# Optimization experiments

Hardware: AMD Instinct MI355X
Metric: run time of the kernel (lower is better)

The kernel has to match this reference:

```python
import jax, jax.numpy as jnp
import numpy as np

B, C, LEN_TS = 4096, 8, 1024
DIM = 2               # shapelet_info[5]
START, END = 0, 628   # max(100-128,0), min(500+128,1024)
L = 64                # len_shapelet
E = 128               # shape_embed_dim
NORM = 1000.0
MAX_CI = 3.0


def setup_inputs() -> dict:
    key = jax.random.key(0)
    k = jax.random.split(key, 6)
    x = jax.random.normal(k[0], (B, C, LEN_TS), dtype=jnp.float32)
    shapelet = jax.random.normal(k[1], (L,), dtype=jnp.float32)
    W1 = jax.random.normal(k[2], (E, L), dtype=jnp.float32) * 0.1
    b1 = jax.random.normal(k[3], (E,), dtype=jnp.float32) * 0.1
    W2 = jax.random.normal(k[4], (E, L), dtype=jnp.float32) * 0.1
    b2 = jax.random.normal(k[5], (E,), dtype=jnp.float32) * 0.1
    return {"x": x, "shapelet": shapelet, "W1": W1, "b1": b1, "W2": W2, "b2": b2}


def reference(x, shapelet, W1, b1, W2, b2):
    piss = x[:, DIM, START:END]                      # [B, T], T = 628
    T = END - START
    NW = T - L + 1                                   # 565 windows

    # squared first differences, then sliding sums of length L-1 via cumsum
    d2 = jnp.square(piss[:, 1:] - piss[:, :-1])      # [B, T-1]
    cs = jnp.concatenate([jnp.zeros((piss.shape[0], 1), piss.dtype),
                          jnp.cumsum(d2, axis=1)], axis=1)   # [B, T]
    piss_ci = jnp.sqrt(cs[:, L - 1:] - cs[:, :NW] + 1.0 / NORM)  # [B, NW]

    # shapelet complexity (constant at init in torch: computed with numpy)
    s_ci = jax.lax.stop_gradient(
        jnp.sqrt(jnp.sum(jnp.square(shapelet[1:] - shapelet[:-1])) + 1.0 / NORM))

    CF = jnp.minimum(jnp.maximum(piss_ci, s_ci) / jnp.minimum(piss_ci, s_ci), MAX_CI)

    # sliding windows [B, NW, L]
    idx = jnp.arange(NW)[:, None] + jnp.arange(L)[None, :]
    piss_w = piss[:, idx]

    ED = jnp.sqrt(jnp.sum(jnp.square(piss_w - shapelet[None, None, :]), axis=-1))  # [B, NW]
    CID = ED * CF

    index = jnp.argmin(CID, axis=1)                  # [B]
    out_i = jnp.take_along_axis(piss_w, index[:, None, None], axis=1)[:, 0, :]  # [B, L]

    out_i = out_i @ W1.T + b1                        # [B, E]
    out_s = shapelet @ W2.T + b2                     # [E]
    out = out_i - out_s[None, :]
    return out.reshape(piss.shape[0], 1, -1)
```

## Files before the change

kernel.cpp:

```cpp
#include <hip/hip_runtime.h>
#include <math.h>

#define NB      4096
#define T       628
#define LW      64
#define NW      565
#define EW      128
#define XSTRIDE 8192
#define XOFF    2048
#define WPT     5

#define WS_SCI 128
#define WS_SS2 129
#define WS_W1T 132
#define WS_NEEDED ((WS_W1T + EW * LW) * sizeof(float))

__global__ __launch_bounds__(64) void prep_kernel(
        const float* __restrict__ shapelet,
        const float* __restrict__ b1,
        const float* __restrict__ W1,
        const float* __restrict__ W2,
        const float* __restrict__ b2,
        float* __restrict__ ws, int use_wt) {
    const int b = blockIdx.x;
    const int j = threadIdx.x;
    const float sh = shapelet[j];
    if (b < EW) {
        const int e = b;
        float dot = sh * W2[e * LW + j];
        #pragma unroll
        for (int off = 32; off; off >>= 1) dot += __shfl_xor(dot, off, 64);
        if (use_wt) ws[WS_W1T + j * EW + e] = W1[e * LW + j];
        if (j == 0) ws[e] = b1[e] - (dot + b2[e]);
    } else {
        float shn = __shfl_down(sh, 1, 64);
        float d = (j < LW - 1) ? (shn - sh) * (shn - sh) : 0.f;
        float q = sh * sh;
        #pragma unroll
        for (int off = 32; off; off >>= 1) {
            d += __shfl_xor(d, off, 64);
            q += __shfl_xor(q, off, 64);
        }
        if (j == 0) { ws[WS_SCI] = sqrtf(d + 0.001f); ws[WS_SS2] = q; }
    }
}

__global__ __launch_bounds__(128, 8) void shapeblock_kernel(
        const float* __restrict__ x,
        const float* __restrict__ shapelet,
        const float* __restrict__ W1,
        const float* __restrict__ ws,
        float* __restrict__ out, int use_wt) {
    __shared__ __align__(16) float sp[T];
    __shared__ unsigned long long red[2];

    const int b   = blockIdx.x;
    const int tid = threadIdx.x;

    const float4* xr4 = (const float4*)(x + (size_t)b * XSTRIDE + XOFF);
    float4* sp4 = (float4*)sp;
    sp4[tid] = xr4[tid];
    if (tid < T / 4 - 128) sp4[tid + 128] = xr4[tid + 128];
    const float s_ci = ws[WS_SCI];
    const float ss2  = ws[WS_SS2];
    __syncthreads();

    const int w0 = (tid * WPT < NW) ? tid * WPT : 0;

    float ring[WPT], acc[WPT], head[WPT];
    #pragma unroll
    for (int i = 0; i < WPT; ++i) {
        ring[i] = sp[w0 + i];
        head[i] = ring[i];
        acc[i]  = 0.f;
    }
    float sd = 0.f, sw2 = 0.f, prev = 0.f;
    #pragma unroll
    for (int j = 0; j < LW; ++j) {
        const float sj = shapelet[j];
        const float v  = ring[j % WPT];
        sw2 = fmaf(v, v, sw2);
        if (j > 0) { float d = v - prev; sd = fmaf(d, d, sd); }
        prev = v;
        #pragma unroll
        for (int i = 0; i < WPT; ++i)
            acc[i] = fmaf(ring[(j + i) % WPT], sj, acc[i]);
        if (j < LW - 1) ring[j % WPT] = sp[w0 + j + WPT];
    }

    unsigned long long key = ~0ull;
    #pragma unroll
    for (int k = 0; k < WPT; ++k) {
        const int w = w0 + k;
        float pci = sqrtf(sd + 0.001f);
        float ed  = sqrtf(fmaxf(fmaf(-2.f, acc[k], sw2 + ss2), 0.f));
        float cf  = fminf(fmaxf(pci, s_ci) / fminf(pci, s_ci), 3.0f);
        float cid = ed * cf;
        unsigned long long kk =
            ((unsigned long long)__float_as_uint(cid) << 32) | (unsigned)w;
        key = kk < key ? kk : key;
        if (k < WPT - 1) {
            float dold = head[k + 1] - head[k];
            float dnew = ring[(4 + k) % WPT] - ring[(3 + k) % WPT];
            sd  = fmaf(dnew, dnew, fmaf(-dold, dold, sd));
            float vold = head[k], vnew = ring[(4 + k) % WPT];
            sw2 = fmaf(vnew, vnew, fmaf(-vold, vold, sw2));
        }
    }

    #pragma unroll
    for (int off = 32; off; off >>= 1) {
        unsigned long long o =
            (unsigned long long)__shfl_xor((long long)key, off, 64);
        key = o < key ? o : key;
    }
    if ((tid & 63) == 0) red[tid >> 6] = key;
    __syncthreads();
    unsigned long long k0 = red[0], k1 = red[1];
    const int widx = (int)((k0 < k1 ? k0 : k1) & 0xffffffffu);

    float a0 = ws[tid];
    if (use_wt) {
        const float* wt = ws + WS_W1T;
        #pragma unroll
        for (int j = 0; j < LW; ++j)
            a0 = fmaf(sp[widx + j], wt[j * EW + tid], a0);
    } else {
        #pragma unroll
        for (int j = 0; j < LW; ++j)
            a0 = fmaf(sp[widx + j], W1[tid * LW + j], a0);
    }
    out[(size_t)b * EW + tid] = a0;
}

extern "C" void kernel_launch(void* const* d_in, const int* in_sizes, int n_in,
                              void* d_out, int out_size, void* d_ws, size_t ws_size,
                              hipStream_t stream) {
    const float* x        = (const float*)d_in[0];
    const float* shapelet = (const float*)d_in[1];
    const float* W1       = (const float*)d_in[2];
    const float* b1       = (const float*)d_in[3];
    const float* W2       = (const float*)d_in[4];
    const float* b2       = (const float*)d_in[5];
    float* out = (float*)d_out;
    float* ws  = (float*)d_ws;

    const int use_wt = (ws_size >= WS_NEEDED) ? 1 : 0;

    prep_kernel<<<EW + 1, 64, 0, stream>>>(shapelet, b1, W1, W2, b2, ws, use_wt);
    shapeblock_kernel<<<NB, 128, 0, stream>>>(x, shapelet, W1, ws, out, use_wt);
}
```

Measured before the change: 25.93 us.

## Fuse prep kernel into main kernel and process two rows per block

Removes the separate prep kernel: each block now computes the shapelet complexity and squared norm in registers, and one half of the block computes the W2·shapelet bias term while the other half does the W1 projection. Blocks grow to 256 threads and handle two batch rows, so the W1 row loaded as float4 is reused for both rows. This drops one kernel launch and the workspace round-trip. In exchange, every block redoes the W2 dot products, and W1 is read in its untransposed layout, which is strided across threads.

```diff
diff --git a/kernel.cpp b/kernel.cpp
--- a/kernel.cpp
+++ b/kernel.cpp
@@ -10,67 +10,49 @@
 #define XOFF    2048
 #define WPT     5
 
-#define WS_SCI 128
-#define WS_SS2 129
-#define WS_W1T 132
-#define WS_NEEDED ((WS_W1T + EW * LW) * sizeof(float))
-
-__global__ __launch_bounds__(64) void prep_kernel(
-        const float* __restrict__ shapelet,
-        const float* __restrict__ b1,
-        const float* __restrict__ W1,
-        const float* __restrict__ W2,
-        const float* __restrict__ b2,
-        float* __restrict__ ws, int use_wt) {
-    const int b = blockIdx.x;
-    const int j = threadIdx.x;
-    const float sh = shapelet[j];
-    if (b < EW) {
-        const int e = b;
-        float dot = sh * W2[e * LW + j];
-        #pragma unroll
-        for (int off = 32; off; off >>= 1) dot += __shfl_xor(dot, off, 64);
-        if (use_wt) ws[WS_W1T + j * EW + e] = W1[e * LW + j];
-        if (j == 0) ws[e] = b1[e] - (dot + b2[e]);
-    } else {
-        float shn = __shfl_down(sh, 1, 64);
-        float d = (j < LW - 1) ? (shn - sh) * (shn - sh) : 0.f;
-        float q = sh * sh;
-        #pragma unroll
-        for (int off = 32; off; off >>= 1) {
-            d += __shfl_xor(d, off, 64);
-            q += __shfl_xor(q, off, 64);
-        }
-        if (j == 0) { ws[WS_SCI] = sqrtf(d + 0.001f); ws[WS_SS2] = q; }
-    }
-}
-
-__global__ __launch_bounds__(128, 8) void shapeblock_kernel(
+__global__ __launch_bounds__(256, 8) void shapeblock_fused(
         const float* __restrict__ x,
         const float* __restrict__ shapelet,
         const float* __restrict__ W1,
-        const float* __restrict__ ws,
-        float* __restrict__ out, int use_wt) {
-    __shared__ __align__(16) float sp[T];
-    __shared__ unsigned long long red[2];
+        const float* __restrict__ b1,
+        const float* __restrict__ W2,
+        const float* __restrict__ b2,
+        float* __restrict__ out) {
+    __shared__ __align__(16) float sp[2][T];
+    __shared__ unsigned long long red[4];
+    __shared__ float s2dot[EW];
 
-    const int b   = blockIdx.x;
-    const int tid = threadIdx.x;
+    const int tid  = threadIdx.x;
+    const int half = tid >> 7;
+    const int l    = tid & 127;
+    const int lane = tid & 63;
+    const int row0 = blockIdx.x * 2;
 
-    const float4* xr4 = (const float4*)(x + (size_t)b * XSTRIDE + XOFF);
-    float4* sp4 = (float4*)sp;
-    sp4[tid] = xr4[tid];
-    if (tid < T / 4 - 128) sp4[tid + 128] = xr4[tid + 128];
-    const float s_ci = ws[WS_SCI];
-    const float ss2  = ws[WS_SS2];
+    const float4* xr4 = (const float4*)(x + (size_t)(row0 + half) * XSTRIDE + XOFF);
+    float4* sp4 = (float4*)sp[half];
+    sp4[l] = xr4[l];
+    if (l < T / 4 - 128) sp4[l + 128] = xr4[l + 128];
+
+    const float shv = shapelet[lane];
+    float shn = __shfl_down(shv, 1, 64);
+    float dsum = (lane < LW - 1) ? (shn - shv) * (shn - shv) : 0.f;
+    float qsum = shv * shv;
+    #pragma unroll
+    for (int off = 32; off; off >>= 1) {
+        dsum += __shfl_xor(dsum, off, 64);
+        qsum += __shfl_xor(qsum, off, 64);
+    }
+    const float s_ci = sqrtf(dsum + 0.001f);
+    const float ss2  = qsum;
     __syncthreads();
 
-    const int w0 = (tid * WPT < NW) ? tid * WPT : 0;
+    const float* mysp = sp[half];
+    const int w0 = (l * WPT < NW) ? l * WPT : 0;
 
     float ring[WPT], acc[WPT], head[WPT];
     #pragma unroll
     for (int i = 0; i < WPT; ++i) {
-        ring[i] = sp[w0 + i];
+        ring[i] = mysp[w0 + i];
         head[i] = ring[i];
         acc[i]  = 0.f;
     }
@@ -85,7 +67,7 @@
         #pragma unroll
         for (int i = 0; i < WPT; ++i)
             acc[i] = fmaf(ring[(j + i) % WPT], sj, acc[i]);
-        if (j < LW - 1) ring[j % WPT] = sp[w0 + j + WPT];
+        if (j < LW - 1) ring[j % WPT] = mysp[w0 + j + WPT];
     }
 
     unsigned long long key = ~0ull;
@@ -114,23 +96,49 @@
             (unsigned long long)__shfl_xor((long long)key, off, 64);
         key = o < key ? o : key;
     }
-    if ((tid & 63) == 0) red[tid >> 6] = key;
+    if (lane == 0) red[tid >> 6] = key;
     __syncthreads();
-    unsigned long long k0 = red[0], k1 = red[1];
-    const int widx = (int)((k0 < k1 ? k0 : k1) & 0xffffffffu);
+    unsigned long long r0 = red[0], r1 = red[1], r2 = red[2], r3 = red[3];
+    const int widx0 = (int)((r0 < r1 ? r0 : r1) & 0xffffffffu);
+    const int widx1 = (int)((r2 < r3 ? r2 : r3) & 0xffffffffu);
 
-    float a0 = ws[tid];
-    if (use_wt) {
-        const float* wt = ws + WS_W1T;
+    float a0 = 0.f, a1 = 0.f;
+    if (half == 0) {
+        const float4* w1r = (const float4*)(W1 + l * LW);
         #pragma unroll
-        for (int j = 0; j < LW; ++j)
-            a0 = fmaf(sp[widx + j], wt[j * EW + tid], a0);
+        for (int k = 0; k < LW / 4; ++k) {
+            float4 wv = w1r[k];
+            const int j = 4 * k;
+            a0 = fmaf(sp[0][widx0 + j    ], wv.x, a0);
+            a0 = fmaf(sp[0][widx0 + j + 1], wv.y, a0);
+            a0 = fmaf(sp[0][widx0 + j + 2], wv.z, a0);
+            a0 = fmaf(sp[0][widx0 + j + 3], wv.w, a0);
+            a1 = fmaf(sp[1][widx1 + j    ], wv.x, a1);
+            a1 = fmaf(sp[1][widx1 + j + 1], wv.y, a1);
+            a1 = fmaf(sp[1][widx1 + j + 2], wv.z, a1);
+            a1 = fmaf(sp[1][widx1 + j + 3], wv.w, a1);
+        }
     } else {
+        const float4* w2r = (const float4*)(W2 + l * LW);
+        float d = 0.f;
         #pragma unroll
-        for (int j = 0; j < LW; ++j)
-            a0 = fmaf(sp[widx + j], W1[tid * LW + j], a0);
+        for (int k = 0; k < LW / 4; ++k) {
+            float4 wv = w2r[k];
+            const int j = 4 * k;
+            d = fmaf(shapelet[j    ], wv.x, d);
+            d = fmaf(shapelet[j + 1], wv.y, d);
+            d = fmaf(shapelet[j + 2], wv.z, d);
+            d = fmaf(shapelet[j + 3], wv.w, d);
+        }
+        s2dot[l] = d;
     }
-    out[(size_t)b * EW + tid] = a0;
+    __syncthreads();
+
+    if (half == 0) {
+        const float bias = b1[l] - b2[l] - s2dot[l];
+        out[(size_t)row0 * EW + l]       = a0 + bias;
+        out[(size_t)(row0 + 1) * EW + l] = a1 + bias;
+    }
 }
 
 extern "C" void kernel_launch(void* const* d_in, const int* in_sizes, int n_in,
@@ -143,10 +151,6 @@
     const float* W2       = (const float*)d_in[4];
     const float* b2       = (const float*)d_in[5];
     float* out = (float*)d_out;
-    float* ws  = (float*)d_ws;
 
-    const int use_wt = (ws_size >= WS_NEEDED) ? 1 : 0;
-
-    prep_kernel<<<EW + 1, 64, 0, stream>>>(shapelet, b1, W1, W2, b2, ws, use_wt);
-    shapeblock_kernel<<<NB, 128, 0, stream>>>(x, shapelet, W1, ws, out, use_wt);
+    shapeblock_fused<<<NB / 2, 256, 0, stream>>>(x, shapelet, W1, b1, W2, b2, out);
 }
```

After: 23.82 us. -8.1%, faster.
